# Performance work log

Hardware: AMD Instinct MI355X
Metric: run time of the kernel (lower is better)

The kernel has to match this reference:

```python
import jax, jax.numpy as jnp
import numpy as np

BN_EPS = 1e-5

def _bn_relu(x, gamma, beta):
    # training-mode BatchNorm1d: biased batch stats over (B, N) per channel
    mean = x.mean(axis=(0, 2), keepdims=True)
    var = x.var(axis=(0, 2), keepdims=True)
    xn = (x - mean) * jax.lax.rsqrt(var + BN_EPS)
    return jax.nn.relu(xn * gamma[None, :, None] + beta[None, :, None])


def setup_inputs() -> dict:
    key = jax.random.key(0)
    ks = jax.random.split(key, 12)
    B, n1, n2, c1, c2 = 16, 4096, 1024, 128, 256
    in_ch, mlp = c1 + c2, [256, 128]
    xyz1 = jax.random.uniform(ks[0], (B, n1, 3), dtype=jnp.float32)
    xyz2 = jax.random.uniform(ks[1], (B, n2, 3), dtype=jnp.float32)
    feat1 = jax.random.normal(ks[2], (B, c1, n1), dtype=jnp.float32)
    feat2 = jax.random.normal(ks[3], (B, c2, n2), dtype=jnp.float32)
    # Conv1d(k=1) weights as (out, in) matrices; kaiming-ish scale
    w0 = jax.random.normal(ks[4], (mlp[0], in_ch), dtype=jnp.float32) / np.sqrt(in_ch)
    b0 = jnp.zeros((mlp[0],), jnp.float32)
    g0 = jnp.ones((mlp[0],), jnp.float32)
    be0 = jnp.zeros((mlp[0],), jnp.float32)
    w1 = jax.random.normal(ks[5], (mlp[1], mlp[0]), dtype=jnp.float32) / np.sqrt(mlp[0])
    b1 = jnp.zeros((mlp[1],), jnp.float32)
    g1 = jnp.ones((mlp[1],), jnp.float32)
    be1 = jnp.zeros((mlp[1],), jnp.float32)
    return {"xyz1": xyz1, "xyz2": xyz2, "feat1": feat1, "feat2": feat2,
            "w0": w0, "b0": b0, "g0": g0, "be0": be0,
            "w1": w1, "b1": b1, "g1": g1, "be1": be1}


def reference(xyz1, xyz2, feat1, feat2, w0, b0, g0, be0, w1, b1, g1, be1):
    # three_nn_interpolate: squared pairwise dists (B, n1, n2)
    d = jnp.sum((xyz1[:, :, None, :] - xyz2[:, None, :, :]) ** 2, axis=-1)
    neg_d3, idx3 = jax.lax.top_k(-d, 3)          # 3 smallest dists
    d3 = -neg_d3                                  # (B, n1, 3)
    w = 1.0 / (d3 + 1e-8)
    w = w / jnp.sum(w, axis=-1, keepdims=True)
    # gather feat2 at knn indices: (B, c2, n1, 3)
    gathered = jnp.take_along_axis(feat2[:, :, None, :], idx3[:, None, :, :], axis=3)
    interp = jnp.sum(gathered * w[:, None, :, :], axis=-1)  # (B, c2, n1)

    x = jnp.concatenate([feat1, interp], axis=1)            # (B, c1+c2, n1)
    x = _bn_relu(jnp.einsum('oc,bcn->bon', w0, x) + b0[None, :, None], g0, be0)
    x = _bn_relu(jnp.einsum('oc,bcn->bon', w1, x) + b1[None, :, None], g1, be1)
    return x
```

## Files before the change

kernel.cpp:

```cpp
#include <hip/hip_runtime.h>
#include <hip/hip_bf16.h>

typedef unsigned short u16;
typedef __attribute__((ext_vector_type(8))) __bf16 bf16x8;
typedef __attribute__((ext_vector_type(4))) float floatx4;

#define B_   16
#define N1_  4096
#define N2_  1024
#define C1_  128
#define C2_  256
#define CIN_ 384
#define CM_  256
#define CO_  128

__device__ __forceinline__ u16 f2bf(float f) {
  unsigned u = __float_as_uint(f);
  u = (u + 0x7fffu + ((u >> 16) & 1u)) >> 16;
  return (u16)u;
}
__device__ __forceinline__ float bf2f(u16 h) {
  return __uint_as_float(((unsigned)h) << 16);
}

union U128 { uint4 u; bf16x8 v; u16 s[8]; };

__device__ __forceinline__ bf16x8 ldfrag(const u16* p) {
  U128 x; x.u = *(const uint4*)p; return x.v;
}
__device__ __forceinline__ uint4 pack8(const u16* h) {
  uint4 u;
  u.x = (unsigned)h[0] | ((unsigned)h[1] << 16);
  u.y = (unsigned)h[2] | ((unsigned)h[3] << 16);
  u.z = (unsigned)h[4] | ((unsigned)h[5] << 16);
  u.w = (unsigned)h[6] | ((unsigned)h[7] << 16);
  return u;
}


__global__ __launch_bounds__(256) void knn_part_kernel(
    const float* __restrict__ xyz1, const float* __restrict__ xyz2,
    float* __restrict__ pd, int* __restrict__ pi,
    const float* __restrict__ w0, const float* __restrict__ w1,
    u16* __restrict__ w0b, u16* __restrict__ w1b)
{
  __shared__ float4 sp[128];
  int t = threadIdx.x;
  if (blockIdx.x == 16) {
    int item = (blockIdx.y * 8 + blockIdx.z) * 256 + t;
    if (item < 12288) {
      int m = item / 48, kc = item % 48;
      const float* p = w0 + m * CIN_ + kc * 8;
      u16 h8[8];
      #pragma unroll
      for (int j = 0; j < 8; ++j) h8[j] = f2bf(p[j]);
      int mt = m >> 4, col = m & 15, kt = kc >> 2, quad = kc & 3;
      *(uint4*)(w0b + ((mt*12 + kt)*512 + (quad*16 + col)*8)) = pack8(h8);
    } else if (item < 16384) {
      int i2 = item - 12288;
      int m = i2 >> 5, kc = i2 & 31;
      const float* p = w1 + m * CM_ + kc * 8;
      u16 h8[8];
      #pragma unroll
      for (int j = 0; j < 8; ++j) h8[j] = f2bf(p[j]);
      int mt = m >> 4, col = m & 15, kt = kc >> 2, quad = kc & 3;
      *(uint4*)(w1b + ((mt*8 + kt)*512 + (quad*16 + col)*8)) = pack8(h8);
    }
    return;
  }
  int b = blockIdx.y, chunk = blockIdx.z;
  const float* p2 = xyz2 + ((size_t)b * N2_ + chunk * 128) * 3;
  if (t < 128) sp[t] = make_float4(p2[t*3], p2[t*3+1], p2[t*3+2], 0.f);
  __syncthreads();
  int i = blockIdx.x * 256 + t;
  const float* p1 = xyz1 + ((size_t)b * N1_ + i) * 3;
  float x = p1[0], y = p1[1], z = p1[2];
  float d0 = 1e30f, d1 = 1e30f, d2 = 1e30f;
  int i0 = 0, i1 = 0, i2 = 0;
  int jb = chunk * 128;
  #pragma unroll 4
  for (int j = 0; j < 128; ++j) {
    float4 p = sp[j];
    float dx = x - p.x, dy = y - p.y, dz = z - p.z;
    float d = dx*dx + dy*dy + dz*dz;
    if (d < d2) {
      int jj = jb + j;
      if (d < d0)      { d2=d1; i2=i1; d1=d0; i1=i0; d0=d; i0=jj; }
      else if (d < d1) { d2=d1; i2=i1; d1=d;  i1=jj; }
      else             { d2=d;  i2=jj; }
    }
  }
  int o = chunk*65536 + b*4096 + i;
  pd[o] = d0; pd[o + 524288] = d1; pd[o + 1048576] = d2;
  pi[o] = i0; pi[o + 524288] = i1; pi[o + 1048576] = i2;
}

__global__ __launch_bounds__(256) void tr2m_kernel(
    const float* __restrict__ feat2, u16* __restrict__ feat2Tb,
    const float* __restrict__ pd, const int* __restrict__ pi,
    int* __restrict__ idx_out, float* __restrict__ w_out)
{
  __shared__ float sA[64][257];
  int t = threadIdx.x;
  if (blockIdx.x >= 16) {
    int p = (blockIdx.y * 16 + (blockIdx.x - 16)) * 256 + t;
    float d0 = 1e30f, d1 = 1e30f, d2 = 1e30f;
    int i0 = 0, i1 = 0, i2 = 0;
    #pragma unroll
    for (int c = 0; c < 8; ++c) {
      int o = c*65536 + p;
      #pragma unroll
      for (int k = 0; k < 3; ++k) {
        float d = pd[o + k*524288];
        int ix = pi[o + k*524288];
        bool c2 = d < d2, c1 = d < d1, c0 = d < d0;
        d2 = c1 ? d1 : (c2 ? d  : d2);
        i2 = c1 ? i1 : (c2 ? ix : i2);
        d1 = c0 ? d0 : (c1 ? d  : d1);
        i1 = c0 ? i0 : (c1 ? ix : i1);
        d0 = c0 ? d  : d0;
        i0 = c0 ? ix : i0;
      }
    }
    float w0 = 1.f/(d0+1e-8f), w1 = 1.f/(d1+1e-8f), w2 = 1.f/(d2+1e-8f);
    float inv = 1.f/(w0+w1+w2);
    idx_out[p]          = i0;
    idx_out[p +  65536] = i1;
    idx_out[p + 131072] = i2;
    w_out[p]            = w0*inv;
    w_out[p +  65536]   = w1*inv;
    w_out[p + 131072]   = w2*inv;
    return;
  }
  int b = blockIdx.y;
  int n0 = blockIdx.x * 64;
  #pragma unroll
  for (int j = 0; j < 16; ++j) {
    int flat4 = t + j * 256;
    int c = flat4 >> 4, nn4 = (flat4 & 15) * 4;
    float4 v = *(const float4*)(feat2 + ((size_t)b*C2_ + c)*N2_ + n0 + nn4);
    sA[nn4+0][c] = v.x; sA[nn4+1][c] = v.y; sA[nn4+2][c] = v.z; sA[nn4+3][c] = v.w;
  }
  __syncthreads();
  int nn = t & 63, chunk = t >> 6;
  u16* dst = feat2Tb + ((size_t)b*N2_ + n0 + nn)*C2_ + chunk*64;
  #pragma unroll
  for (int g = 0; g < 8; ++g) {
    u16 h8[8];
    #pragma unroll
    for (int j = 0; j < 8; ++j) h8[j] = f2bf(sA[nn][chunk*64 + g*8 + j]);
    *(uint4*)(dst + g*8) = pack8(h8);
  }
}

__global__ __launch_bounds__(256) void prep_fused_kernel(
    const float* __restrict__ feat1, const u16* __restrict__ feat2Tb,
    const int* __restrict__ idx_in, const float* __restrict__ w_in,
    u16* __restrict__ xcatT)
{
  __shared__ float sA[64][133];
  int b = blockIdx.y;
  int t = threadIdx.x;
  if (blockIdx.x < 64) {
    int n0 = blockIdx.x * 64;
    #pragma unroll
    for (int j = 0; j < 8; ++j) {
      int flat4 = t + j * 256;
      int c = flat4 >> 4, nn4 = (flat4 & 15) * 4;
      float4 v = *(const float4*)(feat1 + ((size_t)b*C1_ + c)*N1_ + n0 + nn4);
      sA[nn4+0][c] = v.x; sA[nn4+1][c] = v.y; sA[nn4+2][c] = v.z; sA[nn4+3][c] = v.w;
    }
    __syncthreads();
    int nn = t & 63, chunk = t >> 6;
    int n = n0 + nn, nt = n >> 4, col = n & 15;
    u16* tb = xcatT + ((size_t)b*256 + nt)*12*512;
    #pragma unroll
    for (int g = 0; g < 4; ++g) {
      int c0 = chunk*32 + g*8;
      u16 h8[8];
      #pragma unroll
      for (int j = 0; j < 8; ++j) h8[j] = f2bf(sA[nn][c0 + j]);
      *(uint4*)(tb + (size_t)chunk*512 + (g*16 + col)*8) = pack8(h8);
    }
  } else {
    int p0 = (blockIdx.x - 64) * 64;
    int seg = t & 31;
    int pl  = t >> 5;
    #pragma unroll 2
    for (int pass = 0; pass < 8; ++pass) {
      int n = p0 + pass*8 + pl;
      int base = b*N1_ + n;
      int i0 = idx_in[base], i1 = idx_in[base + 65536], i2 = idx_in[base + 131072];
      float w0 = w_in[base], w1 = w_in[base + 65536], w2 = w_in[base + 131072];
      const u16* fb = feat2Tb + (size_t)b*N2_*C2_ + seg*8;
      U128 a, c, d;
      a.u = *(const uint4*)(fb + (size_t)i0*C2_);
      c.u = *(const uint4*)(fb + (size_t)i1*C2_);
      d.u = *(const uint4*)(fb + (size_t)i2*C2_);
      u16 h8[8];
      #pragma unroll
      for (int j = 0; j < 8; ++j)
        h8[j] = f2bf(w0*bf2f(a.s[j]) + w1*bf2f(c.s[j]) + w2*bf2f(d.s[j]));
      int nt = n >> 4, col = n & 15;
      int kt = 4 + (seg >> 2), quad = seg & 3;
      *(uint4*)(xcatT + (((size_t)b*256 + nt)*12 + kt)*512 + (quad*16 + col)*8) = pack8(h8);
    }
  }
}

__global__ __launch_bounds__(64) void gemm1_mfma(
    const u16* __restrict__ xcatT, const u16* __restrict__ w0b,
    const float* __restrict__ b0p, u16* __restrict__ y0T,
    float* __restrict__ p0)
{
  __shared__ u16 sbuf[2][12][512];
  int lane = threadIdx.x;
  int col = lane & 15, quad = lane >> 4;
  int mb = blockIdx.x;
  int gnb = blockIdx.y;
  int b = gnb >> 6;
  int ntb4 = (gnb & 63) * 4;

  const u16* src[12];
  #pragma unroll
  for (int i = 0; i < 12; ++i)
    src[i] = (i < 8)
      ? (w0b + (size_t)((mb*8 + i) * 12) * 512 + lane*8)
      : (xcatT + (size_t)((b*256 + ntb4 + (i-8)) * 12) * 512 + lane*8);

  floatx4 acc[8][4] = {};

  #pragma unroll
  for (int i = 0; i < 12; ++i)
    __builtin_amdgcn_global_load_lds(
        (const __attribute__((address_space(1))) void*)(src[i]),
        (__attribute__((address_space(3))) void*)(&sbuf[0][i][0]), 16, 0, 0);
  __syncthreads();

  int cur = 0;
  #pragma unroll 1
  for (int kt = 0; kt < 12; ++kt) {
    if (kt < 11) {
      #pragma unroll
      for (int i = 0; i < 12; ++i)
        __builtin_amdgcn_global_load_lds(
            (const __attribute__((address_space(1))) void*)(src[i] + (size_t)(kt+1)*512),
            (__attribute__((address_space(3))) void*)(&sbuf[cur^1][i][0]), 16, 0, 0);
    }
    bf16x8 af[8], bfr[4];
    #pragma unroll
    for (int i = 0; i < 8; ++i) af[i] = ldfrag(&sbuf[cur][i][lane*8]);
    #pragma unroll
    for (int j = 0; j < 4; ++j) bfr[j] = ldfrag(&sbuf[cur][8 + j][lane*8]);
    #pragma unroll
    for (int mt = 0; mt < 8; ++mt)
      #pragma unroll
      for (int nt = 0; nt < 4; ++nt)
        acc[mt][nt] = __builtin_amdgcn_mfma_f32_16x16x32_bf16(af[mt], bfr[nt], acc[mt][nt], 0, 0, 0);
    __syncthreads();
    cur ^= 1;
  }

  int m0 = mb * 128;
  #pragma unroll
  for (int mt = 0; mt < 8; ++mt) {
    float4 bias4 = *(const float4*)(b0p + m0 + mt*16 + quad*4);
    float bia[4] = {bias4.x, bias4.y, bias4.z, bias4.w};
    int kt_out = mb*4 + (mt >> 1);
    int quad_out = ((mt & 1) << 1) | (quad >> 1);
    int j0 = (quad & 1) * 4;
    float s[4] = {}, q[4] = {};
    #pragma unroll
    for (int nt = 0; nt < 4; ++nt) {
      u16 h[4];
      #pragma unroll
      for (int r = 0; r < 4; ++r) {
        float v = acc[mt][nt][r] + bia[r];
        u16 hh = f2bf(v);
        float vr = bf2f(hh);
        h[r] = hh; s[r] += vr; q[r] += vr*vr;
      }
      *(ushort4*)(y0T + (((size_t)b*256 + ntb4 + nt)*8 + kt_out)*512 + (quad_out*16 + col)*8 + j0)
          = make_ushort4(h[0], h[1], h[2], h[3]);
    }
    #pragma unroll
    for (int r = 0; r < 4; ++r) {
      float ss = s[r], qq = q[r];
      #pragma unroll
      for (int msk = 1; msk < 16; msk <<= 1) { ss += __shfl_xor(ss, msk); qq += __shfl_xor(qq, msk); }
      if (col == 0)
        *(float2*)(p0 + ((size_t)(mb*128 + mt*16 + quad*4 + r) * 1024 + gnb) * 2)
            = make_float2(ss, qq);
    }
  }
}

__global__ __launch_bounds__(256) void stats_kernel(
    const float* __restrict__ p, const float* __restrict__ g,
    const float* __restrict__ be, float* __restrict__ scale,
    float* __restrict__ shift)
{
  int c = blockIdx.x, t = threadIdx.x;
  const float* base = p + (size_t)c * 2048;
  float s = 0.f, q = 0.f;
  #pragma unroll
  for (int i = 0; i < 4; ++i) {
    float2 v = *(const float2*)(base + (size_t)(t + i*256) * 2);
    s += v.x; q += v.y;
  }
  #pragma unroll
  for (int m = 1; m < 64; m <<= 1) { s += __shfl_xor(s, m); q += __shfl_xor(q, m); }
  __shared__ float2 red[4];
  if ((t & 63) == 0) red[t >> 6] = make_float2(s, q);
  __syncthreads();
  if (t == 0) {
    float ss = red[0].x + red[1].x + red[2].x + red[3].x;
    float qq = red[0].y + red[1].y + red[2].y + red[3].y;
    float mu  = ss * (1.f/65536.f);
    float var = qq * (1.f/65536.f) - mu*mu;
    float a = g[c] * rsqrtf(var + 1e-5f);
    scale[c] = a; shift[c] = be[c] - mu*a;
  }
}

__global__ __launch_bounds__(64) void gemm2_mfma(
    const u16* __restrict__ y0T, const u16* __restrict__ w1b,
    const float* __restrict__ b1p,
    const float* __restrict__ scale0, const float* __restrict__ shift0,
    float* __restrict__ out, float* __restrict__ p1)
{
  __shared__ u16 sbuf[2][12][512];
  __shared__ float a0s[CM_], bb0s[CM_];
  int lane = threadIdx.x;
  int col = lane & 15, quad = lane >> 4;
  int gnb = blockIdx.x;
  int b = gnb >> 6;
  int ntb4 = (gnb & 63) * 4;

  *(float4*)&a0s[lane*4]  = *(const float4*)(scale0 + lane*4);
  *(float4*)&bb0s[lane*4] = *(const float4*)(shift0 + lane*4);

  const u16* src[12];
  #pragma unroll
  for (int i = 0; i < 12; ++i)
    src[i] = (i < 8)
      ? (w1b + (size_t)(i * 8) * 512 + lane*8)
      : (y0T + (size_t)((b*256 + ntb4 + (i-8)) * 8) * 512 + lane*8);

  floatx4 acc[8][4] = {};

  #pragma unroll
  for (int i = 0; i < 12; ++i)
    __builtin_amdgcn_global_load_lds(
        (const __attribute__((address_space(1))) void*)(src[i]),
        (__attribute__((address_space(3))) void*)(&sbuf[0][i][0]), 16, 0, 0);
  __syncthreads();

  int cur = 0;
  #pragma unroll 1
  for (int kt = 0; kt < 8; ++kt) {
    if (kt < 7) {
      #pragma unroll
      for (int i = 0; i < 12; ++i)
        __builtin_amdgcn_global_load_lds(
            (const __attribute__((address_space(1))) void*)(src[i] + (size_t)(kt+1)*512),
            (__attribute__((address_space(3))) void*)(&sbuf[cur^1][i][0]), 16, 0, 0);
    }
    bf16x8 af[8]; U128 braw[4];
    #pragma unroll
    for (int i = 0; i < 8; ++i) af[i] = ldfrag(&sbuf[cur][i][lane*8]);
    #pragma unroll
    for (int j = 0; j < 4; ++j) braw[j].u = *(const uint4*)(&sbuf[cur][8 + j][lane*8]);
    int c0 = kt*32 + quad*8;
    float av[8], bv[8];
    *(float4*)&av[0] = *(const float4*)&a0s[c0];  *(float4*)&av[4] = *(const float4*)&a0s[c0+4];
    *(float4*)&bv[0] = *(const float4*)&bb0s[c0]; *(float4*)&bv[4] = *(const float4*)&bb0s[c0+4];
    bf16x8 bfv[4];
    #pragma unroll
    for (int j = 0; j < 4; ++j) {
      u16 h8[8];
      #pragma unroll
      for (int e = 0; e < 8; ++e)
        h8[e] = f2bf(fmaxf(fmaf(bf2f(braw[j].s[e]), av[e], bv[e]), 0.f));
      U128 x; x.u = pack8(h8); bfv[j] = x.v;
    }
    #pragma unroll
    for (int mt = 0; mt < 8; ++mt)
      #pragma unroll
      for (int nt = 0; nt < 4; ++nt)
        acc[mt][nt] = __builtin_amdgcn_mfma_f32_16x16x32_bf16(af[mt], bfv[nt], acc[mt][nt], 0, 0, 0);
    __syncthreads();
    cur ^= 1;
  }

  #pragma unroll
  for (int mt = 0; mt < 8; ++mt) {
    float4 bias4 = *(const float4*)(b1p + mt*16 + quad*4);
    float bia[4] = {bias4.x, bias4.y, bias4.z, bias4.w};
    float s[4] = {}, q[4] = {};
    #pragma unroll
    for (int nt = 0; nt < 4; ++nt) {
      int n = ntb4*16 + nt*16 + col;
      #pragma unroll
      for (int r = 0; r < 4; ++r) {
        float v = acc[mt][nt][r] + bia[r];
        out[((size_t)b*CO_ + mt*16 + quad*4 + r)*N1_ + n] = v;
        s[r] += v; q[r] += v*v;
      }
    }
    #pragma unroll
    for (int r = 0; r < 4; ++r) {
      float ss = s[r], qq = q[r];
      #pragma unroll
      for (int msk = 1; msk < 16; msk <<= 1) { ss += __shfl_xor(ss, msk); qq += __shfl_xor(qq, msk); }
      if (col == 0)
        *(float2*)(p1 + ((size_t)(mt*16 + quad*4 + r) * 1024 + gnb) * 2)
            = make_float2(ss, qq);
    }
  }
}

__global__ __launch_bounds__(256) void bnrelu_kernel(
    float* __restrict__ out, const float* __restrict__ scale1, const float* __restrict__ shift1)
{
  int idx = blockIdx.x * 256 + threadIdx.x;
  int c = (idx >> 10) & (CO_ - 1);
  float a = scale1[c];
  float bb = shift1[c];
  float4 v = ((const float4*)out)[idx];
  v.x = fmaxf(fmaf(v.x, a, bb), 0.f);
  v.y = fmaxf(fmaf(v.y, a, bb), 0.f);
  v.z = fmaxf(fmaf(v.z, a, bb), 0.f);
  v.w = fmaxf(fmaf(v.w, a, bb), 0.f);
  ((float4*)out)[idx] = v;
}

extern "C" void kernel_launch(void* const* d_in, const int* in_sizes, int n_in,
                              void* d_out, int out_size, void* d_ws, size_t ws_size,
                              hipStream_t stream)
{
  const float* xyz1  = (const float*)d_in[0];
  const float* xyz2  = (const float*)d_in[1];
  const float* feat1 = (const float*)d_in[2];
  const float* feat2 = (const float*)d_in[3];
  const float* w0    = (const float*)d_in[4];
  const float* b0    = (const float*)d_in[5];
  const float* g0    = (const float*)d_in[6];
  const float* be0   = (const float*)d_in[7];
  const float* w1    = (const float*)d_in[8];
  const float* b1    = (const float*)d_in[9];
  const float* g1    = (const float*)d_in[10];
  const float* be1   = (const float*)d_in[11];
  float* out = (float*)d_out;
  char* ws = (char*)d_ws;

  u16*   xcatT   = (u16*)ws;
  float* knn_pd  = (float*)ws;
  float* p1      = (float*)ws;
  int*   knn_pi  = (int*)(ws + 6291456);
  u16*   y0T     = (u16*)(ws + 50331648);
  u16*   feat2Tb = (u16*)(ws + 50331648);
  u16*   w0b     = (u16*)(ws + 83886080);
  u16*   w1b     = (u16*)(ws + 84082688);
  int*   idx_buf = (int*)(ws + 84148224);
  float* w_buf   = (float*)(ws + 84934656);
  float* p0      = (float*)(ws + 84148224);
  float* scale0  = (float*)(ws + 87293952);
  float* shift0  = scale0 + 256;
  float* scale1  = scale0 + 512;
  float* shift1  = scale0 + 640;

  knn_part_kernel <<<dim3(17,16,8),   256, 0, stream>>>(xyz1, xyz2, knn_pd, knn_pi, w0, w1, w0b, w1b);
  tr2m_kernel     <<<dim3(32,16),     256, 0, stream>>>(feat2, feat2Tb, knn_pd, knn_pi, idx_buf, w_buf);
  prep_fused_kernel<<<dim3(128,16),   256, 0, stream>>>(feat1, feat2Tb, idx_buf, w_buf, xcatT);
  gemm1_mfma      <<<dim3(2,1024),     64, 0, stream>>>(xcatT, w0b, b0, y0T, p0);
  stats_kernel    <<<256,             256, 0, stream>>>(p0, g0, be0, scale0, shift0);
  gemm2_mfma      <<<1024,             64, 0, stream>>>(y0T, w1b, b1, scale0, shift0, out, p1);
  stats_kernel    <<<128,             256, 0, stream>>>(p1, g1, be1, scale1, shift1);
  bnrelu_kernel   <<<8192,            256, 0, stream>>>(out, scale1, shift1);
}
```

Before: 256.5 us.

## Deepen GEMM LDS pipelines to four stages with vmcnt waits instead of barriers

Both MFMA GEMM kernels now use a 4-buffer LDS ring with three tiles prefetched ahead, in place of double buffering. Per-iteration __syncthreads are replaced by explicit s_waitcnt vmcnt counts, which is valid because each block is a single wave. The goal is to hide global-load latency and drop barrier overhead. LDS use doubles, which may reduce occupancy, and correctness now depends on the hand-set vmcnt counts matching the number of outstanding loads.

New measurement: 285.8 us. 1.11x slower.

```diff
diff --git a/kernel.cpp b/kernel.cpp
--- a/kernel.cpp
+++ b/kernel.cpp
@@ -36,6 +36,9 @@
   u.w = (unsigned)h[6] | ((unsigned)h[7] << 16);
   return u;
 }
+
+#define WAITVM(N) do { asm volatile("s_waitcnt vmcnt(" #N ")" ::: "memory"); \
+                       __builtin_amdgcn_sched_barrier(0); } while (0)
 
 
 __global__ __launch_bounds__(256) void knn_part_kernel(
@@ -213,7 +216,7 @@
     const float* __restrict__ b0p, u16* __restrict__ y0T,
     float* __restrict__ p0)
 {
-  __shared__ u16 sbuf[2][12][512];
+  __shared__ u16 sbuf[4][12][512];
   int lane = threadIdx.x;
   int col = lane & 15, quad = lane >> 4;
   int mb = blockIdx.x;
@@ -231,34 +234,36 @@
   floatx4 acc[8][4] = {};
 
   #pragma unroll
-  for (int i = 0; i < 12; ++i)
-    __builtin_amdgcn_global_load_lds(
-        (const __attribute__((address_space(1))) void*)(src[i]),
-        (__attribute__((address_space(3))) void*)(&sbuf[0][i][0]), 16, 0, 0);
-  __syncthreads();
-
-  int cur = 0;
+  for (int s = 0; s < 3; ++s)
+    #pragma unroll
+    for (int i = 0; i < 12; ++i)
+      __builtin_amdgcn_global_load_lds(
+          (const __attribute__((address_space(1))) void*)(src[i] + (size_t)s*512),
+          (__attribute__((address_space(3))) void*)(&sbuf[s][i][0]), 16, 0, 0);
+
   #pragma unroll 1
   for (int kt = 0; kt < 12; ++kt) {
-    if (kt < 11) {
+    if (kt <= 8) {
       #pragma unroll
       for (int i = 0; i < 12; ++i)
         __builtin_amdgcn_global_load_lds(
-            (const __attribute__((address_space(1))) void*)(src[i] + (size_t)(kt+1)*512),
-            (__attribute__((address_space(3))) void*)(&sbuf[cur^1][i][0]), 16, 0, 0);
-    }
+            (const __attribute__((address_space(1))) void*)(src[i] + (size_t)(kt+3)*512),
+            (__attribute__((address_space(3))) void*)(&sbuf[(kt+3)&3][i][0]), 16, 0, 0);
+      WAITVM(36);
+    } else if (kt == 9)  { WAITVM(24); }
+    else if (kt == 10)   { WAITVM(12); }
+    else                 { WAITVM(0);  }
+    const u16* cb = &sbuf[kt & 3][0][0];
     bf16x8 af[8], bfr[4];
     #pragma unroll
-    for (int i = 0; i < 8; ++i) af[i] = ldfrag(&sbuf[cur][i][lane*8]);
-    #pragma unroll
-    for (int j = 0; j < 4; ++j) bfr[j] = ldfrag(&sbuf[cur][8 + j][lane*8]);
+    for (int i = 0; i < 8; ++i) af[i] = ldfrag(cb + i*512 + lane*8);
+    #pragma unroll
+    for (int j = 0; j < 4; ++j) bfr[j] = ldfrag(cb + (8+j)*512 + lane*8);
     #pragma unroll
     for (int mt = 0; mt < 8; ++mt)
       #pragma unroll
       for (int nt = 0; nt < 4; ++nt)
         acc[mt][nt] = __builtin_amdgcn_mfma_f32_16x16x32_bf16(af[mt], bfr[nt], acc[mt][nt], 0, 0, 0);
-    __syncthreads();
-    cur ^= 1;
   }
 
   int m0 = mb * 128;
@@ -329,7 +334,7 @@
     const float* __restrict__ scale0, const float* __restrict__ shift0,
     float* __restrict__ out, float* __restrict__ p1)
 {
-  __shared__ u16 sbuf[2][12][512];
+  __shared__ u16 sbuf[4][12][512];
   __shared__ float a0s[CM_], bb0s[CM_];
   int lane = threadIdx.x;
   int col = lane & 15, quad = lane >> 4;
@@ -350,27 +355,33 @@
   floatx4 acc[8][4] = {};
 
   #pragma unroll
-  for (int i = 0; i < 12; ++i)
-    __builtin_amdgcn_global_load_lds(
-        (const __attribute__((address_space(1))) void*)(src[i]),
-        (__attribute__((address_space(3))) void*)(&sbuf[0][i][0]), 16, 0, 0);
-  __syncthreads();
-
-  int cur = 0;
+  for (int s = 0; s < 3; ++s)
+    #pragma unroll
+    for (int i = 0; i < 12; ++i)
+      __builtin_amdgcn_global_load_lds(
+          (const __attribute__((address_space(1))) void*)(src[i] + (size_t)s*512),
+          (__attribute__((address_space(3))) void*)(&sbuf[s][i][0]), 16, 0, 0);
+  asm volatile("s_waitcnt lgkmcnt(0)" ::: "memory");
+  __builtin_amdgcn_sched_barrier(0);
+
   #pragma unroll 1
   for (int kt = 0; kt < 8; ++kt) {
-    if (kt < 7) {
+    if (kt <= 4) {
       #pragma unroll
       for (int i = 0; i < 12; ++i)
         __builtin_amdgcn_global_load_lds(
-            (const __attribute__((address_space(1))) void*)(src[i] + (size_t)(kt+1)*512),
-            (__attribute__((address_space(3))) void*)(&sbuf[cur^1][i][0]), 16, 0, 0);
-    }
+            (const __attribute__((address_space(1))) void*)(src[i] + (size_t)(kt+3)*512),
+            (__attribute__((address_space(3))) void*)(&sbuf[(kt+3)&3][i][0]), 16, 0, 0);
+      WAITVM(36);
+    } else if (kt == 5) { WAITVM(24); }
+    else if (kt == 6)   { WAITVM(12); }
+    else                { WAITVM(0);  }
+    const u16* cb = &sbuf[kt & 3][0][0];
     bf16x8 af[8]; U128 braw[4];
     #pragma unroll
-    for (int i = 0; i < 8; ++i) af[i] = ldfrag(&sbuf[cur][i][lane*8]);
-    #pragma unroll
-    for (int j = 0; j < 4; ++j) braw[j].u = *(const uint4*)(&sbuf[cur][8 + j][lane*8]);
+    for (int i = 0; i < 8; ++i) af[i] = ldfrag(cb + i*512 + lane*8);
+    #pragma unroll
+    for (int j = 0; j < 4; ++j) braw[j].u = *(const uint4*)(cb + (8+j)*512 + lane*8);
     int c0 = kt*32 + quad*8;
     float av[8], bv[8];
     *(float4*)&av[0] = *(const float4*)&a0s[c0];  *(float4*)&av[4] = *(const float4*)&a0s[c0+4];
@@ -389,8 +400,6 @@
       #pragma unroll
       for (int nt = 0; nt < 4; ++nt)
         acc[mt][nt] = __builtin_amdgcn_mfma_f32_16x16x32_bf16(af[mt], bfv[nt], acc[mt][nt], 0, 0, 0);
-    __syncthreads();
-    cur ^= 1;
   }
 
   #pragma unroll
```
